# Kernel optimization log

Hardware: AMD Instinct MI355X
Metric: run time of the kernel (lower is better)

Reference implementation:

```python
import jax, jax.numpy as jnp
import numpy as np
from functools import partial

DIM, HID, DK, NH, SEQ, B = 1024, 512, 512, 4, 16, 2048
DH = DK // NH  # per-head dim = 128
EPS = 1e-5


def _ln(x, g, b):
    m = x.mean(-1, keepdims=True)
    v = ((x - m) ** 2).mean(-1, keepdims=True)
    return (x - m) * jax.lax.rsqrt(v + EPS) * g + b


def setup_inputs() -> dict:
    key = jax.random.key(0)
    ks = jax.random.split(key, 32)
    it = iter(range(32))
    n = lambda shape, s: jax.random.normal(ks[next(it)], shape, jnp.float32) * s
    inp = {
        'visual': n((B, SEQ, DIM), 1.0),
        'text':   n((B, SEQ, DIM), 1.0),
        'user':   n((B, SEQ, DIM), 1.0),
        'cat':    n((B, SEQ, DIM), 1.0),
        'label':  n((B, SEQ, 1), 1.0),
        'h0':     n((B, HID), 1.0),
        'c0':     n((B, HID), 1.0),
        # fusion MLP: Linear(4*dim -> dim)
        'fus_W': n((DIM, 4 * DIM), 1.0 / np.sqrt(4 * DIM)),
        'fus_b': n((DIM,), 0.01),
        # LayerNormLSTM cell params (gate order i,f,g,o)
        'W_ih': n((4 * HID, DIM), 1.0 / np.sqrt(DIM)),
        'W_hh': n((4 * HID, HID), 1.0 / np.sqrt(HID)),
        'g_ih': 1.0 + n((4 * HID,), 0.1), 'b_ih': n((4 * HID,), 0.01),
        'g_hh': 1.0 + n((4 * HID,), 0.1), 'b_hh': n((4 * HID,), 0.01),
        'g_c':  1.0 + n((HID,), 0.1),     'b_c':  n((HID,), 0.01),
        # attention projections
        'wq_W': n((DK, HID), 1.0 / np.sqrt(HID)), 'wq_b': n((DK,), 0.01),
        'wk_W': n((DK, HID), 1.0 / np.sqrt(HID)), 'wk_b': n((DK,), 0.01),
        'wv_W': n((NH, DK, HID), 1.0 / np.sqrt(HID)), 'wv_b': n((NH, DK), 0.01),
        'wout_W': n((DK, DK * NH), 1.0 / np.sqrt(DK * NH)), 'wout_b': n((DK,), 0.01),
        'out_W': n((1, DK), 1.0 / np.sqrt(DK)), 'out_b': n((1,), 0.01),
    }
    return inp


def reference(visual, text, user, cat, label, h0, c0, fus_W, fus_b,
              W_ih, W_hh, g_ih, b_ih, g_hh, b_hh, g_c, b_c,
              wq_W, wq_b, wk_W, wk_b, wv_W, wv_b, wout_W, wout_b, out_W, out_b):
    # fusion MLP (dropout is identity at inference)
    mods = jnp.concatenate([visual, text, user, cat], axis=-1)  # [B,S,4*DIM]
    v_t = jax.nn.relu(mods @ fus_W.T + fus_b)                    # [B,S,DIM]

    # LayerNorm-LSTM recurrence over time via scan
    def step(carry, x_t):
        h, c = carry
        gates = _ln(x_t @ W_ih.T, g_ih, b_ih) + _ln(h @ W_hh.T, g_hh, b_hh)
        i, f, g, o = jnp.split(gates, 4, axis=-1)
        c = jax.nn.sigmoid(f) * c + jax.nn.sigmoid(i) * jnp.tanh(g)
        h = jax.nn.sigmoid(o) * jnp.tanh(_ln(c, g_c, b_c))
        return (h, c), h

    (hn, _), hs = jax.lax.scan(step, (h0, c0), jnp.swapaxes(v_t, 0, 1))
    lstm_out = jnp.swapaxes(hs, 0, 1)  # [B,S,HID]

    # multi-head dot self-attention against final hidden state
    q = (hn @ wq_W.T + wq_b).reshape(-1, NH, DH)                    # [B,H,dh]
    k = (lstm_out @ wk_W.T + wk_b).reshape(-1, SEQ, NH, DH)         # [B,S,H,dh]
    scores = jnp.einsum('bshd,bhd->bhs', k, q) / np.sqrt(DH)        # [B,H,S]
    attn = jax.nn.softmax(scores, axis=-1)
    # per-head full-width values: V[b,h,s,k]
    V = jnp.einsum('hkd,bsd->bhsk', wv_W, lstm_out) + wv_b[None, :, None, :]
    ctx = jnp.einsum('bhsk,bhs->bhk', V, attn).reshape(-1, NH * DK)  # [B,H*DK]
    out_h = ctx @ wout_W.T + wout_b                                  # [B,DK]
    output = out_h @ out_W.T + out_b                                 # [B,1]

    label_one = label[:, -1, 0]
    loss = jnp.mean((output.reshape(-1) - label_one) ** 2)
    return loss, output
```

## Files before the change

### kernel.cpp

```cpp
#include <hip/hip_runtime.h>
#include <cstdint>

#define B_SZ 2048
#define SEQ  16
#define DIM  1024
#define HID  512
#define DK   512
#define NH   4
#define DH   128
#define GATE 2048
#define EPSV 1e-5f

typedef __bf16 bf8_t __attribute__((ext_vector_type(8)));
typedef float  f4_t  __attribute__((ext_vector_type(4)));
typedef unsigned short u16x8 __attribute__((ext_vector_type(8)));
typedef unsigned short u16x4 __attribute__((ext_vector_type(4)));

__device__ __forceinline__ unsigned short f2bf(float f){
  __bf16 h = (__bf16)f;
  return __builtin_bit_cast(unsigned short, h);
}
__device__ __forceinline__ float bf2f(unsigned short u){
  return __builtin_bit_cast(float, ((unsigned int)u) << 16);
}
__device__ __forceinline__ float sigm(float x){ return 1.f/(1.f+__expf(-x)); }
__device__ __forceinline__ float tanh_f(float x){ return 1.f - 2.f/(__expf(2.f*x)+1.f); }

__device__ __forceinline__ void gload16(const void* g, void* l){
  __builtin_amdgcn_global_load_lds(
      (const __attribute__((address_space(1))) void*)g,
      (__attribute__((address_space(3))) void*)l, 16, 0, 0);
}

template<bool OUT_BF16, bool BIAS, bool RELU>
__global__ __launch_bounds__(512, 2) void gemm256(
    const unsigned short* __restrict__ A,
    const unsigned short* __restrict__ Bw,
    const float* __restrict__ bias,
    void* __restrict__ Cp,
    int N, int K, int nwg)
{
  __shared__ __align__(16) unsigned short As[2][256*64];
  __shared__ __align__(16) unsigned short Bs[2][256*64];
  const int tid = threadIdx.x, lane = tid & 63, w = tid >> 6;
  const int bid = blockIdx.x;
  const int swz = (bid & 7)*(nwg >> 3) + (bid >> 3);
  const int nx  = N >> 8;
  const int lnx = 31 - __clz(nx);
  const int bm0 = (swz >> lnx) << 8;
  const int bn0 = (swz & (nx-1)) << 8;

  const int r8  = lane >> 3;
  const int gsw = ((lane & 7) ^ r8) * 8;
  const unsigned short* Ab = A  + (size_t)(bm0 + w*32 + r8)*K + gsw;
  const unsigned short* Bb = Bw + (size_t)(bn0 + w*32 + r8)*K + gsw;

  f4_t acc[8][4];
  #pragma unroll
  for (int m=0;m<8;++m)
    #pragma unroll
    for (int n=0;n<4;++n) acc[m][n] = (f4_t)0.f;

  const int fr = lane & 15, kg = lane >> 4;
  const int ra0 = (w & 1)*128, rb0 = (w >> 1)*64;
  const int KT = K >> 6;

  auto stage = [&](int buf, int kt){
    const size_t ko = (size_t)kt*64;
    #pragma unroll
    for (int q=0;q<4;++q){
      gload16(Ab + ko + (size_t)q*8*K, &As[buf][(w*4+q)*512]);
      gload16(Bb + ko + (size_t)q*8*K, &Bs[buf][(w*4+q)*512]);
    }
  };

  stage(0, 0);
  for (int kt=0; kt<KT; ++kt){
    const int cur = kt & 1;
    __builtin_amdgcn_sched_barrier(0);
    if (kt+1 < KT){
      stage(cur^1, kt+1);
      asm volatile("s_waitcnt vmcnt(8)" ::: "memory");
    } else {
      asm volatile("s_waitcnt vmcnt(0)" ::: "memory");
    }
    __builtin_amdgcn_s_barrier();
    bf8_t bfr[4][2];
    #pragma unroll
    for (int n=0;n<4;++n)
      #pragma unroll
      for (int kk=0;kk<2;++kk){
        const int r = rb0 + n*16 + fr;
        bfr[n][kk] = *(const bf8_t*)&Bs[cur][r*64 + (((kk*4+kg) ^ (r&7))*8)];
      }
    #pragma unroll
    for (int half=0; half<2; ++half){
      bf8_t af[4][2];
      #pragma unroll
      for (int mi=0;mi<4;++mi)
        #pragma unroll
        for (int kk=0;kk<2;++kk){
          const int r = ra0 + (half*4+mi)*16 + fr;
          af[mi][kk] = *(const bf8_t*)&As[cur][r*64 + (((kk*4+kg) ^ (r&7))*8)];
        }
      __builtin_amdgcn_s_setprio(1);
      #pragma unroll
      for (int mi=0;mi<4;++mi)
        #pragma unroll
        for (int n=0;n<4;++n)
          #pragma unroll
          for (int kk=0;kk<2;++kk)
            acc[half*4+mi][n] = __builtin_amdgcn_mfma_f32_16x16x32_bf16(
                af[mi][kk], bfr[n][kk], acc[half*4+mi][n], 0,0,0);
      __builtin_amdgcn_s_setprio(0);
    }
    __builtin_amdgcn_s_barrier();
  }

  #pragma unroll
  for (int n=0;n<4;++n){
    const int col = bn0 + rb0 + n*16 + fr;
    float bv = 0.f;
    if constexpr (BIAS) bv = bias[col];
    #pragma unroll
    for (int m=0;m<8;++m){
      #pragma unroll
      for (int j=0;j<4;++j){
        const int row = bm0 + ra0 + m*16 + kg*4 + j;
        float v = acc[m][n][j] + bv;
        if constexpr (RELU) v = fmaxf(v, 0.f);
        if constexpr (OUT_BF16) ((unsigned short*)Cp)[(size_t)row*N + col] = f2bf(v);
        else                    ((float*)Cp)[(size_t)row*N + col] = v;
      }
    }
  }
}

template<bool OUT_BF16, bool BIAS>
__global__ __launch_bounds__(256) void gemm64(
    const unsigned short* __restrict__ A,
    const unsigned short* __restrict__ Bw,
    const float* __restrict__ bias,
    void* __restrict__ Cp,
    int N, int K, int nwg)
{
  __shared__ __align__(16) unsigned short As[64*64];
  __shared__ __align__(16) unsigned short Bs[64*64];
  const int tid = threadIdx.x, lane = tid & 63, wave = tid >> 6;
  const int bid = blockIdx.x;
  const int swz = (bid & 7)*(nwg >> 3) + (bid >> 3);
  const int nx  = N >> 6;
  const int lnx = 31 - __clz(nx);
  const int bm0 = (swz >> lnx) << 6;
  const int bn0 = (swz & (nx-1)) << 6;

  const int r8  = lane >> 3;
  const int gsw = ((lane & 7) ^ r8) * 8;
  const unsigned short* Ab = A  + (size_t)(bm0 + wave*16 + r8)*K + gsw;
  const unsigned short* Bb = Bw + (size_t)(bn0 + wave*16 + r8)*K + gsw;
  unsigned short* la = As + wave*1024;
  unsigned short* lb = Bs + wave*1024;

  f4_t acc[2][2];
  #pragma unroll
  for (int m=0;m<2;++m)
    #pragma unroll
    for (int n=0;n<2;++n) acc[m][n] = (f4_t)0.f;

  const int KT = K >> 6;
  const int fr = lane & 15, kg = lane >> 4;
  const int wm = (wave & 1)*32, wn = (wave >> 1)*32;

  for (int kt = 0; kt < KT; ++kt){
    if (kt) __syncthreads();
    const size_t ko = (size_t)kt*64;
    #pragma unroll
    for (int q = 0; q < 2; ++q){
      gload16(Ab + ko + (size_t)q*8*K, la + q*512);
      gload16(Bb + ko + (size_t)q*8*K, lb + q*512);
    }
    __syncthreads();
    #pragma unroll
    for (int kk = 0; kk < 2; ++kk){
      bf8_t af[2], bf_[2];
      #pragma unroll
      for (int m=0;m<2;++m){
        const int r = wm+m*16+fr;
        af[m]  = *(const bf8_t*)&As[r*64 + (((kk*4+kg) ^ (r&7))*8)];
      }
      #pragma unroll
      for (int n=0;n<2;++n){
        const int r = wn+n*16+fr;
        bf_[n] = *(const bf8_t*)&Bs[r*64 + (((kk*4+kg) ^ (r&7))*8)];
      }
      #pragma unroll
      for (int m=0;m<2;++m)
        #pragma unroll
        for (int n=0;n<2;++n)
          acc[m][n] = __builtin_amdgcn_mfma_f32_16x16x32_bf16(af[m], bf_[n], acc[m][n], 0,0,0);
    }
  }

  #pragma unroll
  for (int n=0;n<2;++n){
    const int col = bn0 + wn + n*16 + fr;
    float bv = 0.f;
    if constexpr (BIAS) bv = bias[col];
    #pragma unroll
    for (int m=0;m<2;++m){
      #pragma unroll
      for (int j=0;j<4;++j){
        const int row = bm0 + wm + m*16 + kg*4 + j;
        float v = acc[m][n][j] + bv;
        if constexpr (OUT_BF16) ((unsigned short*)Cp)[(size_t)row*N + col] = f2bf(v);
        else                    ((float*)Cp)[(size_t)row*N + col] = v;
      }
    }
  }
}

__global__ __launch_bounds__(256) void lstm_step(
  const unsigned short* __restrict__ X, const unsigned short* __restrict__ Gh,
  const float* __restrict__ c_src, float* __restrict__ c_dst,
  const float* __restrict__ g_ih, const float* __restrict__ b_ih,
  const float* __restrict__ g_hh, const float* __restrict__ b_hh,
  const float* __restrict__ g_c,  const float* __restrict__ b_c,
  unsigned short* __restrict__ h_out, unsigned short* __restrict__ lstm_out,
  int t)
{
  const int b = blockIdx.x, tid = threadIdx.x;
  __shared__ float xs[GATE];
  __shared__ float gs[GATE];
  __shared__ float red[32];
  const unsigned short* xrow = X  + ((size_t)b*SEQ + t)*GATE;
  const unsigned short* grow = Gh + (size_t)b*GATE;
  u16x8 xv = *(const u16x8*)&xrow[tid*8];
  u16x8 gv = *(const u16x8*)&grow[tid*8];
  float sx=0,sx2=0,sg=0,sg2=0;
  #pragma unroll
  for (int j=0;j<8;++j){
    float x = bf2f(xv[j]), g = bf2f(gv[j]);
    xs[tid*8+j]=x; gs[tid*8+j]=g;
    sx += x; sx2 += x*x; sg += g; sg2 += g*g;
  }
  #pragma unroll
  for (int m=32;m;m>>=1){
    sx += __shfl_xor(sx,m); sx2 += __shfl_xor(sx2,m);
    sg += __shfl_xor(sg,m); sg2 += __shfl_xor(sg2,m);
  }
  const int w = tid>>6;
  if ((tid&63)==0){ red[w]=sx; red[4+w]=sx2; red[8+w]=sg; red[12+w]=sg2; }
  __syncthreads();
  sx  = red[0]+red[1]+red[2]+red[3];
  sx2 = red[4]+red[5]+red[6]+red[7];
  sg  = red[8]+red[9]+red[10]+red[11];
  sg2 = red[12]+red[13]+red[14]+red[15];
  const float mX = sx*(1.f/GATE), mH = sg*(1.f/GATE);
  const float rX = rsqrtf(sx2*(1.f/GATE)-mX*mX+EPSV);
  const float rH = rsqrtf(sg2*(1.f/GATE)-mH*mH+EPSV);

  float cN[2], xo[2]; float sc=0, sc2=0;
  #pragma unroll
  for (int rep=0;rep<2;++rep){
    const int n = tid + rep*256;
    const int ni=n, nf=n+HID, ng=n+2*HID, no=n+3*HID;
    float gi = (xs[ni]-mX)*rX*g_ih[ni]+b_ih[ni] + (gs[ni]-mH)*rH*g_hh[ni]+b_hh[ni];
    float gf = (xs[nf]-mX)*rX*g_ih[nf]+b_ih[nf] + (gs[nf]-mH)*rH*g_hh[nf]+b_hh[nf];
    float gg = (xs[ng]-mX)*rX*g_ih[ng]+b_ih[ng] + (gs[ng]-mH)*rH*g_hh[ng]+b_hh[ng];
    float go = (xs[no]-mX)*rX*g_ih[no]+b_ih[no] + (gs[no]-mH)*rH*g_hh[no]+b_hh[no];
    float co = c_src[(size_t)b*HID + n];
    float cn = sigm(gf)*co + sigm(gi)*tanh_f(gg);
    cN[rep]=cn; xo[rep]=go;
    sc += cn; sc2 += cn*cn;
  }
  #pragma unroll
  for (int m=32;m;m>>=1){ sc += __shfl_xor(sc,m); sc2 += __shfl_xor(sc2,m); }
  if ((tid&63)==0){ red[16+w]=sc; red[20+w]=sc2; }
  __syncthreads();
  sc  = red[16]+red[17]+red[18]+red[19];
  sc2 = red[20]+red[21]+red[22]+red[23];
  const float mC = sc*(1.f/HID);
  const float rC = rsqrtf(sc2*(1.f/HID)-mC*mC+EPSV);
  #pragma unroll
  for (int rep=0;rep<2;++rep){
    const int n = tid + rep*256;
    float hN = sigm(xo[rep])*tanh_f((cN[rep]-mC)*rC*g_c[n]+b_c[n]);
    c_dst[(size_t)b*HID+n] = cN[rep];
    unsigned short hbv = f2bf(hN);
    h_out[(size_t)b*HID+n] = hbv;
    lstm_out[((size_t)b*SEQ+t)*HID+n] = hbv;
  }
}

__global__ __launch_bounds__(256) void attn_out_k(
  const float* __restrict__ q, const unsigned short* __restrict__ Km,
  const unsigned short* __restrict__ lo_all,
  const float* __restrict__ u, const float* __restrict__ Cc,
  float* __restrict__ out)
{
  const int b = blockIdx.x, tid = threadIdx.x;
  __shared__ float qs[DK];
  __shared__ float sc[NH][SEQ];
  __shared__ float at[NH][SEQ];
  __shared__ float red[4];
  for (int i=tid; i<DK; i+=256) qs[i] = q[(size_t)b*DK + i];
  __syncthreads();
  {
    const int p = tid>>2, sub = tid&3, h = p>>4, s = p&15;
    const unsigned short* krow = Km + ((size_t)b*SEQ + s)*DK + h*DH + sub*32;
    const float* qh = &qs[h*DH + sub*32];
    float part = 0.f;
    #pragma unroll
    for (int c8=0;c8<4;++c8){
      u16x8 kv = *(const u16x8*)(krow + c8*8);
      #pragma unroll
      for (int j=0;j<8;++j) part += qh[c8*8+j]*bf2f(kv[j]);
    }
    part += __shfl_xor(part,1); part += __shfl_xor(part,2);
    if (sub==0) sc[h][s] = part * 0.08838834764831845f;
  }
  __syncthreads();
  if (tid < 64){
    const int h = tid>>4;
    float v = sc[h][tid&15], mx = v;
    #pragma unroll
    for (int m=1;m<16;m<<=1) mx = fmaxf(mx, __shfl_xor(mx,m));
    float e = __expf(v-mx), se = e;
    #pragma unroll
    for (int m=1;m<16;m<<=1) se += __shfl_xor(se,m);
    at[h][tid&15] = e/se;
  }
  __syncthreads();
  float accum = 0.f;
  #pragma unroll
  for (int it=0; it<4; ++it){
    const int idx = it*256 + tid;
    const int h = idx>>8, d0 = (idx&255)*2;
    const unsigned short* lo = lo_all + (size_t)b*SEQ*HID + d0;
    float p0=0.f, p1=0.f;
    #pragma unroll
    for (int s=0;s<16;++s){
      unsigned int pr = *(const unsigned int*)(lo + s*HID);
      float a = at[h][s];
      p0 += a*bf2f((unsigned short)(pr&0xffffu));
      p1 += a*bf2f((unsigned short)(pr>>16));
    }
    accum += u[h*HID+d0]*p0 + u[h*HID+d0+1]*p1;
  }
  #pragma unroll
  for (int m=32;m;m>>=1) accum += __shfl_xor(accum,m);
  if ((tid&63)==0) red[tid>>6] = accum;
  __syncthreads();
  if (tid==0) out[1+b] = red[0]+red[1]+red[2]+red[3] + Cc[0];
}

__global__ __launch_bounds__(256) void loss_k(const float* __restrict__ label, float* __restrict__ out){
  const int tid = threadIdx.x;
  __shared__ float red[4];
  float s = 0.f;
  for (int b=tid; b<B_SZ; b+=256){
    float d = out[1+b] - label[(size_t)b*SEQ + (SEQ-1)];
    s += d*d;
  }
  #pragma unroll
  for (int m=32;m;m>>=1) s += __shfl_xor(s,m);
  if ((tid&63)==0) red[tid>>6]=s;
  __syncthreads();
  if (tid==0) out[0] = (red[0]+red[1]+red[2]+red[3]) * (1.f/B_SZ);
}

__global__ __launch_bounds__(256) void cvt_bf16_k(const float* __restrict__ in, unsigned short* __restrict__ o, int n){
  int i = (blockIdx.x*256 + threadIdx.x)*4;
  if (i < n){
    f4_t v = *(const f4_t*)&in[i];
    u16x4 w;
    #pragma unroll
    for (int j=0;j<4;++j) w[j] = f2bf(v[j]);
    *(u16x4*)&o[i] = w;
  }
}

__global__ __launch_bounds__(256) void cvt4_k(
  const float* __restrict__ v0, const float* __restrict__ v1,
  const float* __restrict__ v2, const float* __restrict__ v3,
  unsigned short* __restrict__ dst)
{
  const int idx = blockIdx.x*256 + threadIdx.x;
  const int src = blockIdx.y;
  const float* s = src==0?v0 : src==1?v1 : src==2?v2 : v3;
  const size_t e0 = (size_t)idx*8;
  const int row = (int)(e0 >> 10);
  const int col = (int)(e0 & 1023);
  f4_t a = *(const f4_t*)&s[e0];
  f4_t b = *(const f4_t*)&s[e0+4];
  u16x8 w;
  #pragma unroll
  for (int j=0;j<4;++j){ w[j]=f2bf(a[j]); w[4+j]=f2bf(b[j]); }
  *(u16x8*)&dst[(size_t)row*4096 + src*1024 + col] = w;
}

__global__ __launch_bounds__(256) void fold_we_k(
  const float* __restrict__ wout_W, const float* __restrict__ out_W, float* __restrict__ we)
{
  const int j = blockIdx.x*256 + threadIdx.x;
  float s=0.f;
  for (int m=0;m<512;++m) s += out_W[m]*wout_W[(size_t)m*2048+j];
  we[j]=s;
}
__global__ __launch_bounds__(256) void fold_u_k(
  const float* __restrict__ we, const float* __restrict__ wv_W, float* __restrict__ u)
{
  const int o = blockIdx.x*256 + threadIdx.x;
  const int h = o>>9, d = o&511;
  const float* wv = wv_W + (size_t)h*262144 + d;
  const float* wp = we + h*512;
  float s=0.f;
  for (int k=0;k<512;++k) s += wp[k]*wv[(size_t)k*512];
  u[o]=s;
}
__global__ __launch_bounds__(256) void fold_c_k(
  const float* __restrict__ we, const float* __restrict__ wv_b,
  const float* __restrict__ out_W, const float* __restrict__ wout_b,
  const float* __restrict__ out_b, float* __restrict__ Cc)
{
  const int tid = threadIdx.x;
  __shared__ float red[4];
  float s=0.f;
  for (int j=tid;j<2048;j+=256) s += we[j]*wv_b[j];
  for (int m=tid;m<512;m+=256)  s += out_W[m]*wout_b[m];
  #pragma unroll
  for (int m=32;m;m>>=1) s += __shfl_xor(s,m);
  if ((tid&63)==0) red[tid>>6]=s;
  __syncthreads();
  if (tid==0) Cc[0] = red[0]+red[1]+red[2]+red[3] + out_b[0];
}

extern "C" void kernel_launch(void* const* d_in, const int* in_sizes, int n_in,
                              void* d_out, int out_size, void* d_ws, size_t ws_size,
                              hipStream_t stream)
{
  const float* visual = (const float*)d_in[0];
  const float* text   = (const float*)d_in[1];
  const float* user_  = (const float*)d_in[2];
  const float* cat_   = (const float*)d_in[3];
  const float* label  = (const float*)d_in[4];
  const float* h0     = (const float*)d_in[5];
  const float* c0     = (const float*)d_in[6];
  const float* fus_W  = (const float*)d_in[7];
  const float* fus_b  = (const float*)d_in[8];
  const float* W_ih   = (const float*)d_in[9];
  const float* W_hh   = (const float*)d_in[10];
  const float* g_ih   = (const float*)d_in[11];
  const float* b_ih   = (const float*)d_in[12];
  const float* g_hh   = (const float*)d_in[13];
  const float* b_hh   = (const float*)d_in[14];
  const float* g_c    = (const float*)d_in[15];
  const float* b_c    = (const float*)d_in[16];
  const float* wq_W   = (const float*)d_in[17];
  const float* wq_b   = (const float*)d_in[18];
  const float* wk_W   = (const float*)d_in[19];
  const float* wk_b   = (const float*)d_in[20];
  const float* wv_W   = (const float*)d_in[21];
  const float* wv_b   = (const float*)d_in[22];
  const float* wout_W = (const float*)d_in[23];
  const float* wout_b = (const float*)d_in[24];
  const float* out_W  = (const float*)d_in[25];
  const float* out_b  = (const float*)d_in[26];
  (void)in_sizes; (void)n_in; (void)out_size; (void)ws_size;

  char* base = (char*)d_ws; size_t off = 0;
  auto alloc = [&](size_t n)->void*{ void* p = base+off; off += n; off = (off+255)&~(size_t)255; return p; };
  unsigned short* modsB = (unsigned short*)alloc((size_t)32768*4096*2);
  unsigned short* X     = modsB;
  unsigned short* vt    = (unsigned short*)alloc((size_t)32768*1024*2);
  unsigned short* Gh    = (unsigned short*)alloc((size_t)2048*2048*2);
  float*          cws   = (float*)         alloc((size_t)2048*512*4);
  unsigned short* hb    = (unsigned short*)alloc((size_t)2048*512*2);
  unsigned short* lo    = (unsigned short*)alloc((size_t)32768*512*2);
  unsigned short* Km    = (unsigned short*)alloc((size_t)32768*512*2);
  float*          qb    = (float*)         alloc((size_t)2048*512*4);
  unsigned short* fusWb = (unsigned short*)alloc((size_t)1024*4096*2);
  unsigned short* Wihb  = (unsigned short*)alloc((size_t)2048*1024*2);
  unsigned short* Whhb  = (unsigned short*)alloc((size_t)2048*512*2);
  unsigned short* wqb   = (unsigned short*)alloc((size_t)512*512*2);
  unsigned short* wkb   = (unsigned short*)alloc((size_t)512*512*2);
  float*          we_ws = (float*)         alloc(2048*4);
  float*          u_ws  = (float*)         alloc(2048*4);
  float*          C_ws  = (float*)         alloc(256);

  cvt4_k<<<dim3(16384,4), dim3(256), 0, stream>>>(visual, text, user_, cat_, modsB);
  cvt_bf16_k<<<dim3(4096), dim3(256), 0, stream>>>(fus_W, fusWb, 1024*4096);
  cvt_bf16_k<<<dim3(2048), dim3(256), 0, stream>>>(W_ih,  Wihb,  2048*1024);
  cvt_bf16_k<<<dim3(1024), dim3(256), 0, stream>>>(W_hh,  Whhb,  2048*512);
  cvt_bf16_k<<<dim3(256),  dim3(256), 0, stream>>>(wq_W,  wqb,   512*512);
  cvt_bf16_k<<<dim3(256),  dim3(256), 0, stream>>>(wk_W,  wkb,   512*512);
  cvt_bf16_k<<<dim3(1024), dim3(256), 0, stream>>>(h0,    hb,    2048*512);
  fold_we_k<<<dim3(8), dim3(256), 0, stream>>>(wout_W, out_W, we_ws);
  fold_u_k <<<dim3(8), dim3(256), 0, stream>>>(we_ws, wv_W, u_ws);
  fold_c_k <<<dim3(1), dim3(256), 0, stream>>>(we_ws, wv_b, out_W, wout_b, out_b, C_ws);

  gemm256<true,true,true><<<dim3(512), dim3(512), 0, stream>>>(
      modsB, fusWb, fus_b, vt, 1024, 4096, 512);
  gemm256<true,false,false><<<dim3(1024), dim3(512), 0, stream>>>(
      vt, Wihb, nullptr, X, 2048, 1024, 1024);

  for (int t=0; t<SEQ; ++t){
    gemm64<true,false><<<dim3(1024), dim3(256), 0, stream>>>(
        hb, Whhb, nullptr, Gh, 2048, 512, 1024);
    lstm_step<<<dim3(2048), dim3(256), 0, stream>>>(
        X, Gh, (t==0 ? c0 : cws), cws, g_ih, b_ih, g_hh, b_hh, g_c, b_c, hb, lo, t);
  }

  gemm64<false,true><<<dim3(256), dim3(256), 0, stream>>>(
      hb, wqb, wq_b, qb, 512, 512, 256);
  gemm256<true,true,false><<<dim3(256), dim3(512), 0, stream>>>(
      lo, wkb, wk_b, Km, 512, 512, 256);

  attn_out_k<<<dim3(2048), dim3(256), 0, stream>>>(qb, Km, lo, u_ws, C_ws, (float*)d_out);
  loss_k<<<dim3(1), dim3(256), 0, stream>>>(label, (float*)d_out);
}
```

Before: 1.080 ms.

## Rework large GEMM into eight-phase interleaved load/MFMA pipeline

Replaces the 256x256 GEMM main loop with an 8-phase schedule. Each phase stages a quarter of the next tile's A or B via global_load_lds, reads LDS fragments and issues a slice of MFMAs, with barriers between slices. This keeps memory traffic and matrix work more evenly overlapped instead of one big stage then compute. It also changes the wave tiling to 2x4 and launch bounds to one block per CU, and reorders workspace allocations. The added barriers and reduced occupancy could hurt if latency hiding was already adequate.

Result: faster. 1.004 ms (-7.0%).

```diff
diff --git a/kernel.cpp b/kernel.cpp
--- a/kernel.cpp
+++ b/kernel.cpp
@@ -33,7 +33,7 @@
 }
 
 template<bool OUT_BF16, bool BIAS, bool RELU>
-__global__ __launch_bounds__(512, 2) void gemm256(
+__global__ __launch_bounds__(512, 1) void gemm8p(
     const unsigned short* __restrict__ A,
     const unsigned short* __restrict__ Bw,
     const float* __restrict__ bias,
@@ -50,10 +50,32 @@
   const int bm0 = (swz >> lnx) << 8;
   const int bn0 = (swz & (nx-1)) << 8;
 
-  const int r8  = lane >> 3;
-  const int gsw = ((lane & 7) ^ r8) * 8;
-  const unsigned short* Ab = A  + (size_t)(bm0 + w*32 + r8)*K + gsw;
-  const unsigned short* Bb = Bw + (size_t)(bn0 + w*32 + r8)*K + gsw;
+  const int l8  = lane >> 3;
+  const int gsw = (lane & 7) ^ l8;
+  const int fr  = lane & 15, kg = lane >> 4;
+  const int wm  = (w >> 2)*128, wn = (w & 3)*64;
+  const int KT  = K >> 6;
+
+  auto stA = [&](int buf, int kt, int h){
+    #pragma unroll
+    for (int c=0;c<2;++c){
+      const int rb = h*128 + c*64 + w*8;
+      gload16(A + (size_t)(bm0 + rb + l8)*K + (size_t)kt*64 + gsw*8, &As[buf][rb*64]);
+    }
+  };
+  auto stB = [&](int buf, int kt, int h){
+    #pragma unroll
+    for (int c=0;c<2;++c){
+      const int rb = h*128 + c*64 + w*8;
+      gload16(Bw + (size_t)(bn0 + rb + l8)*K + (size_t)kt*64 + gsw*8, &Bs[buf][rb*64]);
+    }
+  };
+  auto rdA = [&](int buf, int m, int kk)->bf8_t{
+    return *(const bf8_t*)&As[buf][(wm + m*16 + fr)*64 + (((kk*4+kg) ^ (fr&7))*8)];
+  };
+  auto rdB = [&](int buf, int n, int kk)->bf8_t{
+    return *(const bf8_t*)&Bs[buf][(wn + n*16 + fr)*64 + (((kk*4+kg) ^ (fr&7))*8)];
+  };
 
   f4_t acc[8][4];
   #pragma unroll
@@ -61,72 +83,74 @@
     #pragma unroll
     for (int n=0;n<4;++n) acc[m][n] = (f4_t)0.f;
 
-  const int fr = lane & 15, kg = lane >> 4;
-  const int ra0 = (w & 1)*128, rb0 = (w >> 1)*64;
-  const int KT = K >> 6;
-
-  auto stage = [&](int buf, int kt){
-    const size_t ko = (size_t)kt*64;
-    #pragma unroll
-    for (int q=0;q<4;++q){
-      gload16(Ab + ko + (size_t)q*8*K, &As[buf][(w*4+q)*512]);
-      gload16(Bb + ko + (size_t)q*8*K, &Bs[buf][(w*4+q)*512]);
-    }
-  };
-
-  stage(0, 0);
-  for (int kt=0; kt<KT; ++kt){
-    const int cur = kt & 1;
-    __builtin_amdgcn_sched_barrier(0);
-    if (kt+1 < KT){
-      stage(cur^1, kt+1);
-      asm volatile("s_waitcnt vmcnt(8)" ::: "memory");
-    } else {
-      asm volatile("s_waitcnt vmcnt(0)" ::: "memory");
-    }
-    __builtin_amdgcn_s_barrier();
-    bf8_t bfr[4][2];
-    #pragma unroll
-    for (int n=0;n<4;++n)
-      #pragma unroll
-      for (int kk=0;kk<2;++kk){
-        const int r = rb0 + n*16 + fr;
-        bfr[n][kk] = *(const bf8_t*)&Bs[cur][r*64 + (((kk*4+kg) ^ (r&7))*8)];
-      }
-    #pragma unroll
-    for (int half=0; half<2; ++half){
-      bf8_t af[4][2];
-      #pragma unroll
-      for (int mi=0;mi<4;++mi)
-        #pragma unroll
-        for (int kk=0;kk<2;++kk){
-          const int r = ra0 + (half*4+mi)*16 + fr;
-          af[mi][kk] = *(const bf8_t*)&As[cur][r*64 + (((kk*4+kg) ^ (r&7))*8)];
-        }
-      __builtin_amdgcn_s_setprio(1);
-      #pragma unroll
-      for (int mi=0;mi<4;++mi)
-        #pragma unroll
-        for (int n=0;n<4;++n)
-          #pragma unroll
-          for (int kk=0;kk<2;++kk)
-            acc[half*4+mi][n] = __builtin_amdgcn_mfma_f32_16x16x32_bf16(
-                af[mi][kk], bfr[n][kk], acc[half*4+mi][n], 0,0,0);
-      __builtin_amdgcn_s_setprio(0);
-    }
-    __builtin_amdgcn_s_barrier();
+  bf8_t bfr[4][2];
+
+  auto mfma2 = [&](int m0, const bf8_t a00, const bf8_t a01,
+                   const bf8_t a10, const bf8_t a11){
+    __builtin_amdgcn_s_setprio(1);
+    #pragma unroll
+    for (int n=0;n<4;++n){
+      acc[m0][n]   = __builtin_amdgcn_mfma_f32_16x16x32_bf16(a00, bfr[n][0], acc[m0][n],   0,0,0);
+      acc[m0][n]   = __builtin_amdgcn_mfma_f32_16x16x32_bf16(a01, bfr[n][1], acc[m0][n],   0,0,0);
+      acc[m0+1][n] = __builtin_amdgcn_mfma_f32_16x16x32_bf16(a10, bfr[n][0], acc[m0+1][n], 0,0,0);
+      acc[m0+1][n] = __builtin_amdgcn_mfma_f32_16x16x32_bf16(a11, bfr[n][1], acc[m0+1][n], 0,0,0);
+    }
+    __builtin_amdgcn_s_setprio(0);
+  };
+
+  auto phase12 = [&](int buf, auto&& stg){
+    #pragma unroll
+    for (int n=0;n<4;++n){ bfr[n][0]=rdB(buf,n,0); bfr[n][1]=rdB(buf,n,1); }
+    const bf8_t a00=rdA(buf,0,0), a01=rdA(buf,0,1), a10=rdA(buf,1,0), a11=rdA(buf,1,1);
+    stg();
+    asm volatile("s_barrier" ::: "memory");
+    mfma2(0, a00,a01,a10,a11);
+    asm volatile("s_barrier" ::: "memory");
+  };
+  auto phase4 = [&](int buf, int m0, auto&& stg, bool vm){
+    const bf8_t a00=rdA(buf,m0,0), a01=rdA(buf,m0,1), a10=rdA(buf,m0+1,0), a11=rdA(buf,m0+1,1);
+    stg();
+    if (vm){
+      __builtin_amdgcn_sched_barrier(0);
+      asm volatile("s_waitcnt vmcnt(4)" ::: "memory");
+    }
+    asm volatile("s_barrier" ::: "memory");
+    mfma2(m0, a00,a01,a10,a11);
+    asm volatile("s_barrier" ::: "memory");
+  };
+
+  stA(0,0,0); stA(0,0,1); stB(0,0,0); stB(0,0,1);
+  stB(1,1,0); stB(1,1,1);
+  __builtin_amdgcn_sched_barrier(0);
+  asm volatile("s_waitcnt vmcnt(4)" ::: "memory");
+  asm volatile("s_barrier" ::: "memory");
+
+  const int NIT = KT >> 1;
+  for (int it=0; it<NIT; ++it){
+    const int t0 = 2*it, t1 = t0+1;
+    const int tN  = (t0+2 < KT) ? t0+2 : KT-1;
+    const int tB3 = (t1+2 < KT) ? t1+2 : KT-1;
+
+    phase12(0,      [&]{ stA(1,t1,0);  });
+    phase4 (0, 2,   [&]{ stA(1,t1,1);  }, false);
+    phase4 (0, 4,   [&]{ stB(0,tN,0);  }, false);
+    phase4 (0, 6,   [&]{ stB(0,tN,1);  }, true);
+    phase12(1,      [&]{ stA(0,tN,0);  });
+    phase4 (1, 2,   [&]{ stA(0,tN,1);  }, false);
+    phase4 (1, 4,   [&]{ stB(1,tB3,0); }, false);
+    phase4 (1, 6,   [&]{ stB(1,tB3,1); }, true);
   }
 
   #pragma unroll
   for (int n=0;n<4;++n){
-    const int col = bn0 + rb0 + n*16 + fr;
+    const int col = bn0 + wn + n*16 + fr;
     float bv = 0.f;
     if constexpr (BIAS) bv = bias[col];
     #pragma unroll
     for (int m=0;m<8;++m){
       #pragma unroll
       for (int j=0;j<4;++j){
-        const int row = bm0 + ra0 + m*16 + kg*4 + j;
+        const int row = bm0 + wm + m*16 + kg*4 + j;
         float v = acc[m][n][j] + bv;
         if constexpr (RELU) v = fmaxf(v, 0.f);
         if constexpr (OUT_BF16) ((unsigned short*)Cp)[(size_t)row*N + col] = f2bf(v);
@@ -473,11 +497,11 @@
   unsigned short* modsB = (unsigned short*)alloc((size_t)32768*4096*2);
   unsigned short* X     = modsB;
   unsigned short* vt    = (unsigned short*)alloc((size_t)32768*1024*2);
+  unsigned short* lo    = (unsigned short*)alloc((size_t)32768*512*2);
+  unsigned short* Km    = (unsigned short*)alloc((size_t)32768*512*2);
   unsigned short* Gh    = (unsigned short*)alloc((size_t)2048*2048*2);
   float*          cws   = (float*)         alloc((size_t)2048*512*4);
   unsigned short* hb    = (unsigned short*)alloc((size_t)2048*512*2);
-  unsigned short* lo    = (unsigned short*)alloc((size_t)32768*512*2);
-  unsigned short* Km    = (unsigned short*)alloc((size_t)32768*512*2);
   float*          qb    = (float*)         alloc((size_t)2048*512*4);
   unsigned short* fusWb = (unsigned short*)alloc((size_t)1024*4096*2);
   unsigned short* Wihb  = (unsigned short*)alloc((size_t)2048*1024*2);
@@ -499,9 +523,9 @@
   fold_u_k <<<dim3(8), dim3(256), 0, stream>>>(we_ws, wv_W, u_ws);
   fold_c_k <<<dim3(1), dim3(256), 0, stream>>>(we_ws, wv_b, out_W, wout_b, out_b, C_ws);
 
-  gemm256<true,true,true><<<dim3(512), dim3(512), 0, stream>>>(
+  gemm8p<true,true,true><<<dim3(512), dim3(512), 0, stream>>>(
       modsB, fusWb, fus_b, vt, 1024, 4096, 512);
-  gemm256<true,false,false><<<dim3(1024), dim3(512), 0, stream>>>(
+  gemm8p<true,false,false><<<dim3(1024), dim3(512), 0, stream>>>(
       vt, Wihb, nullptr, X, 2048, 1024, 1024);
 
   for (int t=0; t<SEQ; ++t){
@@ -513,7 +537,7 @@
 
   gemm64<false,true><<<dim3(256), dim3(256), 0, stream>>>(
       hb, wqb, wq_b, qb, 512, 512, 256);
-  gemm256<true,true,false><<<dim3(256), dim3(512), 0, stream>>>(
+  gemm8p<true,true,false><<<dim3(256), dim3(512), 0, stream>>>(
       lo, wkb, wk_b, Km, 512, 512, 256);
 
   attn_out_k<<<dim3(2048), dim3(256), 0, stream>>>(qb, Km, lo, u_ws, C_ws, (float*)d_out);
```
